# Kernel optimization log

Hardware: AMD Instinct MI355X
Metric: run time of the kernel (lower is better)

Reference implementation:

```python
import jax, jax.numpy as jnp
import numpy as np

HIDDEN = 2048
VOCAB = 32768
SEQ = 4608
N_CHUNKS = 9
CAP = 30.0
IGNORE = -100


def setup_inputs() -> dict:
    key = jax.random.key(0)
    k1, k2, k3 = jax.random.split(key, 3)
    weight = (jax.random.normal(k1, (VOCAB, HIDDEN), dtype=jnp.float32) * 0.02).astype(jnp.bfloat16)
    hidden = jax.random.normal(k2, (1, SEQ, HIDDEN), dtype=jnp.float32)
    input_ids = jax.random.randint(k3, (1, SEQ), 0, VOCAB)
    attention_mask = jnp.ones((1, SEQ), dtype=jnp.int32)
    return {"weight": weight, "hidden": hidden, "input_ids": input_ids,
            "attention_mask": attention_mask}


def _build_labels(input_ids, attention_mask):
    # labels[t] = input_ids[t+1], masked-out positions and the final position -> -100
    ids = input_ids[0]
    am = attention_mask[0]
    lab = jnp.where(am[1:] == 0, IGNORE, ids[1:])            # [S-1]
    lab = jnp.concatenate([lab, jnp.full((1,), IGNORE, lab.dtype)])  # [S]
    return lab


def reference(weight, hidden, input_ids, attention_mask):
    labels = _build_labels(input_ids, attention_mask)        # [S]
    x = hidden.reshape(-1, HIDDEN)                           # [S, H] fp32
    chunk = SEQ // N_CHUNKS
    xs = x.reshape(N_CHUNKS, chunk, HIDDEN)
    ls = labels.reshape(N_CHUNKS, chunk)

    wT = weight.T                                            # [H, V] bf16

    def chunk_loss(args):
        xc, lc = args                                        # [c,H], [c]
        # softcapped logits: CAP * tanh((x @ W^T) / CAP), mm in bf16
        t = jnp.tanh((xc.astype(jnp.bfloat16) @ wT) / CAP).astype(jnp.float32)  # [c,V]
        z = CAP * (t - jnp.max(t, axis=1, keepdims=True))    # stable shifted logits
        logp = z - jnp.log(jnp.sum(jnp.exp(z), axis=1, keepdims=True))
        valid = lc != IGNORE
        idx = jnp.where(valid, lc, 0)
        nll = -jnp.take_along_axis(logp, idx[:, None], axis=1)[:, 0]
        return jnp.sum(jnp.where(valid, nll, 0.0))

    losses = jax.lax.map(chunk_loss, (xs, ls))               # [N_CHUNKS]
    return jnp.sum(losses)
```

## Files before the change

kernel.cpp:

```cpp
#include <hip/hip_runtime.h>
#include <hip/hip_bf16.h>
#include <cstdint>

#define S_LEN   4608
#define HID     2048
#define VOCAB_N 32768
#define CAPV    30.0f
#define IGNORE_IDX (-100)
#define NT512   512
#define NKS     64

typedef short bf16x8 __attribute__((ext_vector_type(8)));
typedef float f32x4  __attribute__((ext_vector_type(4)));

__device__ __forceinline__ unsigned short f2bf_rtne(float f) {
    unsigned int u = __float_as_uint(f);
    unsigned int r = u + 0x7fffu + ((u >> 16) & 1u);
    return (unsigned short)(r >> 16);
}
__device__ __forceinline__ float bfr(float f) {
    unsigned int u = __float_as_uint(f);
    unsigned int r = u + 0x7fffu + ((u >> 16) & 1u);
    return __uint_as_float(r & 0xffff0000u);
}
__device__ __forceinline__ float bf_lo(unsigned int u) { return __uint_as_float(u << 16); }
__device__ __forceinline__ float bf_hi(unsigned int u) { return __uint_as_float(u & 0xffff0000u); }
__device__ __forceinline__ float bfdot2(unsigned int x, unsigned int w) {
    return bf_lo(x) * bf_lo(w) + bf_hi(x) * bf_hi(w);
}
__device__ __forceinline__ float softcap_ref(float logit) {
    float lb = bfr(logit);
    float x  = bfr(lb / CAPV);
    float e  = __expf(2.0f * x);
    float t  = bfr((e - 1.0f) / (e + 1.0f));
    return CAPV * t;
}

__global__ void cvt_kernel(const float* __restrict__ h, unsigned short* __restrict__ xb,
                           float* __restrict__ out) {
    if (blockIdx.x == 0 && threadIdx.x == 0) out[0] = 0.0f;
    int i = blockIdx.x * blockDim.x + threadIdx.x;
    float4 v = ((const float4*)h)[i];
    ushort4 o;
    o.x = f2bf_rtne(v.x); o.y = f2bf_rtne(v.y);
    o.z = f2bf_rtne(v.z); o.w = f2bf_rtne(v.w);
    ((ushort4*)xb)[i] = o;
}

__global__ __launch_bounds__(1024, 4)
void gemm_lse_kernel(const unsigned short* __restrict__ X,
                     const unsigned short* __restrict__ W,
                     float* __restrict__ partL) {
    __shared__ __align__(16) unsigned short As[2][256 * 32];
    __shared__ __align__(16) unsigned short Bs[2][256 * 32];

    const int tid  = threadIdx.x;
    const int wid  = tid >> 6;
    const int lane = tid & 63;
    const int wr   = wid >> 2;
    const int wc   = wid & 3;
    const int q    = lane >> 4, l16 = lane & 15;
    const int tileM = blockIdx.x * 256;
    const int tileN = blockIdx.y * 256;

    const int lr = lane >> 2;
    const int cg = (lane & 3) ^ ((lane >> 4) & 3);
    const unsigned short* Ag = X + (size_t)(tileM + wid * 16 + lr) * HID + cg * 8;
    const unsigned short* Wg = W + (size_t)(tileN + wid * 16 + lr) * HID + cg * 8;

    const int swz   = (q ^ (l16 >> 2)) * 8;
    const int abase = (wr * 64 + l16) * 32 + swz;
    const int bbase = (wc * 64 + l16) * 32 + swz;

    f32x4 acc[4][4] = {};

#define STAGE(BUF, T) do {                                                                \
    __builtin_amdgcn_global_load_lds(                                                     \
        (const __attribute__((address_space(1))) void*)(Ag + (size_t)(T) * 32),           \
        (__attribute__((address_space(3))) void*)&As[BUF][wid * 512], 16, 0, 0);          \
    __builtin_amdgcn_global_load_lds(                                                     \
        (const __attribute__((address_space(1))) void*)(Wg + (size_t)(T) * 32),           \
        (__attribute__((address_space(3))) void*)&Bs[BUF][wid * 512], 16, 0, 0);          \
} while (0)

#define COMPUTE(BUF) do {                                                                 \
    bf16x8 av[4], bv[4];                                                                  \
    _Pragma("unroll") for (int f = 0; f < 4; ++f) {                                       \
        av[f] = *(const bf16x8*)&As[BUF][abase + f * 512];                                \
        bv[f] = *(const bf16x8*)&Bs[BUF][bbase + f * 512];                                \
    }                                                                                     \
    _Pragma("unroll") for (int m = 0; m < 4; ++m)                                         \
    _Pragma("unroll") for (int n = 0; n < 4; ++n)                                         \
        acc[m][n] = __builtin_amdgcn_mfma_f32_16x16x32_bf16(av[m], bv[n],                 \
                                                            acc[m][n], 0, 0, 0);          \
} while (0)

    STAGE(0, 0);

    #pragma unroll 1
    for (int t = 0; t < NKS - 2; t += 2) {
        __syncthreads();
        STAGE(1, t + 1);
        COMPUTE(0);
        __syncthreads();
        STAGE(0, t + 2);
        COMPUTE(1);
    }
    __syncthreads();
    STAGE(1, NKS - 1);
    COMPUTE(0);
    __syncthreads();
    COMPUTE(1);

    const int rowbase = tileM + wr * 64;
    const int ntile   = blockIdx.y * 4 + wc;
    #pragma unroll
    for (int m = 0; m < 4; ++m) {
        #pragma unroll
        for (int r = 0; r < 4; ++r) {
            float s = 0.0f;
            #pragma unroll
            for (int n = 0; n < 4; ++n)
                s += __expf(softcap_ref(acc[m][n][r]));
            s += __shfl_xor(s, 1);
            s += __shfl_xor(s, 2);
            s += __shfl_xor(s, 4);
            s += __shfl_xor(s, 8);
            if (l16 == 0)
                partL[(size_t)(rowbase + m * 16 + q * 4 + r) * NT512 + ntile] = s;
        }
    }

#undef STAGE
#undef COMPUTE
}

__global__ void row_reduce_kernel(const unsigned short* __restrict__ X,
                                  const unsigned short* __restrict__ W,
                                  const int* __restrict__ ids,
                                  const int* __restrict__ am,
                                  const float* __restrict__ partL,
                                  float* __restrict__ out) {
    __shared__ float blk[4];
    const int wave = threadIdx.x >> 6;
    const int lane = threadIdx.x & 63;
    const int r = blockIdx.x * 4 + wave;

    int lab = IGNORE_IDX;
    if (r < S_LEN - 1 && am[r + 1] != 0) lab = ids[r + 1];
    const bool valid = (lab >= 0 && lab < VOCAB_N);

    float dot = 0.0f;
    if (valid) {
        const unsigned short* xr = X + (size_t)r   * HID;
        const unsigned short* wr = W + (size_t)lab * HID;
        #pragma unroll
        for (int c = 0; c < 4; ++c) {
            const int off = c * 512 + lane * 8;
            uint4 xu = *(const uint4*)(xr + off);
            uint4 wu = *(const uint4*)(wr + off);
            dot += bfdot2(xu.x, wu.x) + bfdot2(xu.y, wu.y) +
                   bfdot2(xu.z, wu.z) + bfdot2(xu.w, wu.w);
        }
    }
    #pragma unroll
    for (int m = 1; m < 64; m <<= 1) dot += __shfl_xor(dot, m);

    float L = 0.0f;
    const float* pr = partL + (size_t)r * NT512;
    #pragma unroll
    for (int i = 0; i < 8; ++i) L += pr[i * 64 + lane];
    #pragma unroll
    for (int m = 1; m < 64; m <<= 1) L += __shfl_xor(L, m);

    if (lane == 0) {
        float loss = 0.0f;
        if (valid) loss = logf(L) - softcap_ref(dot);
        blk[wave] = loss;
    }
    __syncthreads();
    if (threadIdx.x == 0)
        atomicAdd(out, blk[0] + blk[1] + blk[2] + blk[3]);
}

extern "C" void kernel_launch(void* const* d_in, const int* in_sizes, int n_in,
                              void* d_out, int out_size, void* d_ws, size_t ws_size,
                              hipStream_t stream) {
    const unsigned short* W  = (const unsigned short*)d_in[0];
    const float*  hidden     = (const float*)d_in[1];
    const int*    ids        = (const int*)d_in[2];
    const int*    am         = (const int*)d_in[3];
    float* out = (float*)d_out;

    char* ws = (char*)d_ws;
    unsigned short* Xb = (unsigned short*)ws;
    float* partL       = (float*)(ws + (size_t)S_LEN * HID * 2);

    cvt_kernel<<<(S_LEN * HID / 4) / 256, 256, 0, stream>>>(hidden, Xb, out);

    dim3 g(S_LEN / 256, VOCAB_N / 256);
    gemm_lse_kernel<<<g, 1024, 0, stream>>>(Xb, W, partL);

    row_reduce_kernel<<<S_LEN / 4, 256, 0, stream>>>(Xb, W, ids, am, partL, out);
}
```

Measured before the change: 1.121 ms.

## Schedule GEMM tiles dynamically per XCC partition for L2 locality

Each GEMM block now reads its hardware XCC id and claims a tile from a per-XCC atomic work counter. The 18x128 tile grid is split into 8 quadrant partitions of 9x32 tiles, with work stealing from other partitions once its own is exhausted. The aim is for blocks on the same XCC to share X and W tiles in their private L2, cutting HBM/LLC traffic. The cost is an atomic and a barrier per block, plus counters that cvt_kernel must reset.

```diff
diff --git a/kernel.cpp b/kernel.cpp
--- a/kernel.cpp
+++ b/kernel.cpp
@@ -37,8 +37,11 @@
 }
 
 __global__ void cvt_kernel(const float* __restrict__ h, unsigned short* __restrict__ xb,
-                           float* __restrict__ out) {
-    if (blockIdx.x == 0 && threadIdx.x == 0) out[0] = 0.0f;
+                           float* __restrict__ out, unsigned int* __restrict__ cnt) {
+    if (blockIdx.x == 0) {
+        if (threadIdx.x == 0) out[0] = 0.0f;
+        if (threadIdx.x < 8)  cnt[threadIdx.x] = 0u;
+    }
     int i = blockIdx.x * blockDim.x + threadIdx.x;
     float4 v = ((const float4*)h)[i];
     ushort4 o;
@@ -50,9 +53,11 @@
 __global__ __launch_bounds__(1024, 4)
 void gemm_lse_kernel(const unsigned short* __restrict__ X,
                      const unsigned short* __restrict__ W,
-                     float* __restrict__ partL) {
+                     float* __restrict__ partL,
+                     unsigned int* __restrict__ cnt) {
     __shared__ __align__(16) unsigned short As[2][256 * 32];
     __shared__ __align__(16) unsigned short Bs[2][256 * 32];
+    __shared__ int sh_item;
 
     const int tid  = threadIdx.x;
     const int wid  = tid >> 6;
@@ -60,8 +65,29 @@
     const int wr   = wid >> 2;
     const int wc   = wid & 3;
     const int q    = lane >> 4, l16 = lane & 15;
-    const int tileM = blockIdx.x * 256;
-    const int tileN = blockIdx.y * 256;
+
+    if (tid == 0) {
+        unsigned int xcc;
+        asm volatile("s_getreg_b32 %0, hwreg(HW_REG_XCC_ID)" : "=s"(xcc));
+        xcc &= 7u;
+        int item = -1;
+        #pragma unroll 1
+        for (int p = 0; p < 8 && item < 0; ++p) {
+            unsigned int part = (xcc + p) & 7u;
+            unsigned int c = atomicAdd(&cnt[part], 1u);
+            if (c < 288u) item = (int)(part * 288u + c);
+        }
+        sh_item = item;
+    }
+    __syncthreads();
+    const int item = sh_item;
+    const int part = item / 288, c = item % 288;
+    const int qa = part & 1, qb = part >> 1;
+    const int wy = c / 72, rem = c % 72;
+    const int xt = qa * 9  + rem % 9;
+    const int yt = qb * 32 + wy * 8 + rem / 9;
+    const int tileM = xt * 256;
+    const int tileN = yt * 256;
 
     const int lr = lane >> 2;
     const int cg = (lane & 3) ^ ((lane >> 4) & 3);
@@ -113,7 +139,7 @@
     COMPUTE(1);
 
     const int rowbase = tileM + wr * 64;
-    const int ntile   = blockIdx.y * 4 + wc;
+    const int ntile   = yt * 4 + wc;
     #pragma unroll
     for (int m = 0; m < 4; ++m) {
         #pragma unroll
@@ -195,11 +221,12 @@
     char* ws = (char*)d_ws;
     unsigned short* Xb = (unsigned short*)ws;
     float* partL       = (float*)(ws + (size_t)S_LEN * HID * 2);
-
-    cvt_kernel<<<(S_LEN * HID / 4) / 256, 256, 0, stream>>>(hidden, Xb, out);
-
-    dim3 g(S_LEN / 256, VOCAB_N / 256);
-    gemm_lse_kernel<<<g, 1024, 0, stream>>>(Xb, W, partL);
+    unsigned int* cnt  = (unsigned int*)(ws + (size_t)S_LEN * HID * 2
+                                            + (size_t)S_LEN * NT512 * 4);
+
+    cvt_kernel<<<(S_LEN * HID / 4) / 256, 256, 0, stream>>>(hidden, Xb, out, cnt);
+
+    gemm_lse_kernel<<<(S_LEN / 256) * (VOCAB_N / 256), 1024, 0, stream>>>(Xb, W, partL, cnt);
 
     row_reduce_kernel<<<S_LEN / 4, 256, 0, stream>>>(Xb, W, ids, am, partL, out);
 }
```

After: 1.116 ms. No clear change (-0.4%).
